# Kernel tuning notes

Measured on AMD Instinct MI355X. Metric: run time of the kernel, lower is better.

Reference implementation:

```python
import jax, jax.numpy as jnp
import numpy as np

T = 36
N_POLES = 40
LAM = 0.1
MAX_ITER = 100
TOL = 1e-4
B, P = 2, 4096


def build_dictionary(Drr, Dtheta):
    # rows i = 0..T-1; columns: [rr^i cos(i th), (-rr)^i cos(i th), rr^i sin(i th), (-rr)^i sin(i th)]
    i = jnp.arange(T, dtype=Drr.dtype)[:, None]              # [T,1]
    pr = jnp.power(Drr[None, :], i)                          # rr^i   [T,N]
    sign = jnp.power(jnp.asarray(-1.0, Drr.dtype), i)        # (-1)^i [T,1]
    c = jnp.cos(i * Dtheta[None, :])
    s = jnp.sin(i * Dtheta[None, :])
    dic = jnp.concatenate([pr * c, sign * pr * c, pr * s, sign * pr * s], axis=1)  # [T,4N]
    G = jnp.linalg.norm(dic, axis=0)                         # column norms
    G = jnp.where(G == 0, jnp.sqrt(jnp.asarray(float(T), dic.dtype)), G)
    return dic / G


def soft_shrink(v, lambd):
    return jnp.sign(v) * jnp.maximum(jnp.abs(v) - lambd, 0.0)


def fista(D, Y, lam, max_iter=MAX_ITER):
    DtD = D.T @ D                                            # [4N,4N]
    L = jnp.linalg.norm(DtD)                                 # torch.norm(DtD, 2) = Frobenius norm
    linv = 1.0 / L
    DtY = jnp.einsum('tk,btp->bkp', D, Y) * linv             # [B,4N,P]
    K = DtD.shape[0]
    A = jnp.eye(K, dtype=D.dtype) - DtD * linv               # [4N,4N]
    lambd = lam * linv
    Bb, _, Pp = DtY.shape

    # FISTA momentum coefficients are data independent -> precompute
    ts = np.ones(max_iter + 1)
    for k in range(max_iter):
        ts[k + 1] = (1 + np.sqrt(1 + 4 * ts[k] ** 2)) / 2.0
    tts = jnp.asarray((ts[:-1] - 1) / ts[1:], dtype=D.dtype)  # [max_iter]

    x0 = jnp.zeros((Bb, K, Pp), dtype=D.dtype)

    def step(carry, inputs):
        x_old, y_old, done = carry
        tt, k = inputs
        x_new = soft_shrink(jnp.einsum('kj,bjp->bkp', A, y_old) + DtY, lambd)
        y_new = x_new * (1 + tt) - x_old * tt
        # torch divides by x_old.shape[1]: P on the first check (x_old is the 2-D zeros init), 4N after
        denom = jnp.where(k == 0, float(Pp), float(K)).astype(x_new.dtype)
        conv = jnp.linalg.norm(x_old - x_new) / denom < TOL
        x_out = jnp.where(done, x_old, x_new)
        y_out = jnp.where(done, y_old, y_new)
        return (x_out, y_out, jnp.logical_or(done, conv)), None

    (x_fin, _, _), _ = jax.lax.scan(step, (x0, x0, jnp.array(False)),
                                    (tts, jnp.arange(max_iter)))
    return x_fin


def setup_inputs() -> dict:
    key = jax.random.key(0)
    k1, k2, k3 = jax.random.split(key, 3)
    Drr = jax.random.uniform(k1, (N_POLES,), dtype=jnp.float32)
    Dtheta = jax.random.uniform(k2, (N_POLES,), dtype=jnp.float32)
    x = jax.random.normal(k3, (B, T, P), dtype=jnp.float32)
    return {"Drr": Drr, "Dtheta": Dtheta, "x": x}


def reference(Drr, Dtheta, x):
    dic = build_dictionary(Drr, Dtheta)   # [T, 4N]
    sparsecode = fista(dic, x, LAM)       # [B, 4N, P]
    return sparsecode
```

## Files before the change

kernel.cpp:

```cpp
#include <hip/hip_runtime.h>
#include <hip/hip_bf16.h>
#include <hip/hip_fp16.h>

#define TT 36
#define KK 160
#define NPOLE 40
#define PP 4096
#define MAXIT 100
#define COLS 16
#define NG 2
#define NWC 4
#define NTHR 512
#define YS 168
#define GRID 256

#define WS_LINV  0
#define WS_LAMBD 1
#define WS_TTS   2
#define WS_FROB  132
#define WS_D     512
#define WS_A     6400
#define WS_AH    32000
#define WS_AL    44800

typedef float    floatx4 __attribute__((ext_vector_type(4)));
typedef short    shortx8 __attribute__((ext_vector_type(8)));
typedef _Float16 halfx8  __attribute__((ext_vector_type(8)));

__global__ void setup1(const float* __restrict__ Drr,
                       const float* __restrict__ Dth,
                       float* __restrict__ ws) {
  __shared__ float Dl[TT * KK];
  __shared__ float Gl[KK];
  const int tid = threadIdx.x;
  if (tid == 0) ws[WS_FROB] = 0.f;

  for (int idx = tid; idx < TT * KK; idx += 256) {
    int i = idx / KK, k = idx % KK;
    int g = k / NPOLE, n = k % NPOLE;
    float rr = Drr[n], th = Dth[n];
    float pr = powf(rr, (float)i);
    float ang = (float)i * th;
    float tri = (g < 2) ? cosf(ang) : sinf(ang);
    float sgn = ((g & 1) && (i & 1)) ? -1.0f : 1.0f;
    Dl[idx] = pr * tri * sgn;
  }
  __syncthreads();
  if (tid < KK) {
    float s = 0.f;
    for (int i = 0; i < TT; i++) { float v = Dl[i * KK + tid]; s += v * v; }
    float gn = sqrtf(s);
    Gl[tid] = (gn == 0.f) ? sqrtf((float)TT) : gn;
  }
  __syncthreads();
  for (int idx = tid; idx < TT * KK; idx += 256)
    ws[WS_D + idx] = Dl[idx] / Gl[idx % KK];

  if (tid == 0) {
    double ts = 1.0;
    for (int k = 0; k < MAXIT; k++) {
      double tn = (1.0 + sqrt(1.0 + 4.0 * ts * ts)) * 0.5;
      ws[WS_TTS + k] = (float)((ts - 1.0) / tn);
      ts = tn;
    }
  }
}

__global__ void setup2(float* __restrict__ ws) {
  __shared__ float red[256];
  const int a = blockIdx.x, b = threadIdx.x;
  const float* D = &ws[WS_D];
  float ss = 0.f;
  if (b < KK) {
    float s = 0.f;
    for (int t = 0; t < TT; t++) s += D[t * KK + a] * D[t * KK + b];
    ws[WS_A + a * KK + b] = s;
    ss = s * s;
  }
  red[b] = ss;
  __syncthreads();
  for (int off = 128; off > 0; off >>= 1) {
    if (b < off) red[b] += red[b + off];
    __syncthreads();
  }
  if (b == 0) atomicAdd(&ws[WS_FROB], red[0]);
}

__global__ void setup3(float* __restrict__ ws) {
  const int idx = blockIdx.x * 256 + threadIdx.x;
  const float linv = 1.0f / sqrtf(ws[WS_FROB]);
  _Float16* AHs = (_Float16*)&ws[WS_AH];
  if (idx < KK * KK) {
    int a = idx / KK, b = idx % KK;
    float av = (a == b) ? (1.0f - linv) : (0.0f - ws[WS_A + idx] * linv);
    AHs[idx] = (_Float16)av;
  }
  if (idx == 0) { ws[WS_LINV] = linv; ws[WS_LAMBD] = 0.1f * linv; }
}

__global__ __launch_bounds__(NTHR, 2)
void fista_kernel(const float* __restrict__ x, float* __restrict__ out,
                  float* __restrict__ ws) {
  __shared__ __align__(16) short ys[NG][2][COLS * YS];
  __shared__ float ttsl[MAXIT];
  __shared__ unsigned cnt[NG];

  const int tid  = threadIdx.x;
  const int w    = tid >> 6;
  const int lane = tid & 63;
  const int quad = lane >> 4;
  const int l16  = lane & 15;
  const int g    = w >> 2;
  const int v    = w & 3;
  const int bid  = blockIdx.x;
  const int bb   = (bid * 32) / PP;
  const int p0   = (bid * 32) % PP + 16 * g;
  const float linv  = ws[WS_LINV];
  const float lambd = ws[WS_LAMBD];
  const float adiag = 1.0f - linv;
  const float ahf   = (float)(_Float16)adiag;
  const float ddiag = adiag - ahf;

  int base, nrs;
  if (g == 0) { base = (v < 2) ? 48 * v : 32 * v + 32; nrs = (v < 2) ? 3 : 2; }
  else        { base = (v < 2) ? 32 * v : 48 * v - 32; nrs = (v < 2) ? 2 : 3; }

  for (int i = tid; i < MAXIT; i += NTHR) ttsl[i] = ws[WS_TTS + i];

  const _Float16* AH = (const _Float16*)&ws[WS_AH];
  halfx8 ah[3][5];
#pragma unroll
  for (int rs = 0; rs < 3; rs++) {
    if (rs < nrs) {
#pragma unroll
      for (int kc = 0; kc < 5; kc++) {
        int off = (base + 16 * rs + l16) * KK + 32 * kc + 8 * quad;
        ah[rs][kc] = *(const halfx8*)&AH[off];
      }
    }
  }

  const float* Dg = &ws[WS_D];
  float dty[3][4] = {{0.f,0.f,0.f,0.f},{0.f,0.f,0.f,0.f},{0.f,0.f,0.f,0.f}};
  {
    const float* xcol = &x[(size_t)bb * TT * PP + p0 + l16];
    for (int t = 0; t < TT; t++) {
      float xv = xcol[(size_t)t * PP];
#pragma unroll
      for (int rs = 0; rs < 3; rs++) {
        if (rs < nrs) {
          float4 d = *(const float4*)&Dg[t * KK + base + 16 * rs + 4 * quad];
          dty[rs][0] = fmaf(d.x, xv, dty[rs][0]);
          dty[rs][1] = fmaf(d.y, xv, dty[rs][1]);
          dty[rs][2] = fmaf(d.z, xv, dty[rs][2]);
          dty[rs][3] = fmaf(d.w, xv, dty[rs][3]);
        }
      }
    }
#pragma unroll
    for (int rs = 0; rs < 3; rs++)
#pragma unroll
      for (int r = 0; r < 4; r++) dty[rs][r] *= linv;
  }

  {
    int* z = (int*)&ys[0][0][0];
    for (int i = tid; i < NG * 2 * COLS * YS / 2; i += NTHR) z[i] = 0;
    if (tid < NG) cnt[tid] = 0;
  }
  float xo[3][4] = {{0.f,0.f,0.f,0.f},{0.f,0.f,0.f,0.f},{0.f,0.f,0.f,0.f}};
  float yl[3][4] = {{0.f,0.f,0.f,0.f},{0.f,0.f,0.f,0.f},{0.f,0.f,0.f,0.f}};
  float yv[3][4] = {{0.f,0.f,0.f,0.f},{0.f,0.f,0.f,0.f},{0.f,0.f,0.f,0.f}};
  __syncthreads();

  if (g == 1) __builtin_amdgcn_s_sleep(10);
  __builtin_amdgcn_s_setprio(1);

#define RD_MFMA(KC) { \
    halfx8 bh = *(const halfx8*)&yb[cb + 32 * (KC)]; \
    _Pragma("unroll") \
    for (int rs = 0; rs < 3; rs++) \
      if (rs < nrs) \
        accM[rs] = __builtin_amdgcn_mfma_f32_16x16x32_f16(ah[rs][KC], bh, accM[rs], 0, 0, 0); \
  }

#define ITER_BODY(SK, K1, K2, K3, K4) { \
    RD_MFMA(SK) \
    if (it > 0) { \
      const unsigned tgt = (unsigned)(NWC * it); \
      __builtin_amdgcn_s_setprio(0); \
      while (__atomic_load_n(&cnt[g], __ATOMIC_ACQUIRE) < tgt) \
        __builtin_amdgcn_s_sleep(1); \
      __builtin_amdgcn_s_setprio(1); \
    } \
    RD_MFMA(K1) RD_MFMA(K2) RD_MFMA(K3) RD_MFMA(K4) \
  }

  for (int it = 0; it < MAXIT; it++) {
    const short* yb = &ys[g][it & 1][0];
    const int cb = l16 * YS + 8 * quad;
    floatx4 accM[3] = {{dty[0][0], dty[0][1], dty[0][2], dty[0][3]},
                       {dty[1][0], dty[1][1], dty[1][2], dty[1][3]},
                       {dty[2][0], dty[2][1], dty[2][2], dty[2][3]}};

    if (g == 0) {
      if      (v == 0) ITER_BODY(0, 1, 2, 3, 4)
      else if (v == 1) ITER_BODY(2, 0, 1, 3, 4)
      else if (v == 2) ITER_BODY(3, 0, 1, 2, 4)
      else             ITER_BODY(4, 0, 1, 2, 3)
    } else {
      if      (v == 0) ITER_BODY(0, 1, 2, 3, 4)
      else if (v == 1) ITER_BODY(1, 0, 2, 3, 4)
      else if (v == 2) ITER_BODY(2, 0, 1, 3, 4)
      else             ITER_BODY(4, 0, 1, 2, 3)
    }

    const float tt = ttsl[it];
    short* yw = &ys[g][(it & 1) ^ 1][0];
#pragma unroll
    for (int rs = 0; rs < 3; rs++) {
      if (rs < nrs) {
        float yn[4];
#pragma unroll
        for (int r = 0; r < 4; r++) {
          float vv = fmaf(ddiag, yv[rs][r], fmaf(ahf, yl[rs][r], accM[rs][r]));
          float cl = __builtin_amdgcn_fmed3f(vv, -lambd, lambd);
          float xv = vv - cl;
          yn[r] = fmaf(tt, xv - xo[rs][r], xv);
          xo[rs][r] = xv;
        }
        _Float16 h0 = (_Float16)yn[0], h1 = (_Float16)yn[1];
        _Float16 h2 = (_Float16)yn[2], h3 = (_Float16)yn[3];
        yl[rs][0] = yn[0] - (float)h0;  yv[rs][0] = yn[0];
        yl[rs][1] = yn[1] - (float)h1;  yv[rs][1] = yn[1];
        yl[rs][2] = yn[2] - (float)h2;  yv[rs][2] = yn[2];
        yl[rs][3] = yn[3] - (float)h3;  yv[rs][3] = yn[3];
        unsigned u01 = (unsigned)__builtin_bit_cast(unsigned short, h0) |
                       ((unsigned)__builtin_bit_cast(unsigned short, h1) << 16);
        unsigned u23 = (unsigned)__builtin_bit_cast(unsigned short, h2) |
                       ((unsigned)__builtin_bit_cast(unsigned short, h3) << 16);
        const int ko = l16 * YS + base + 16 * rs + 4 * quad;
        *(uint2*)&yw[ko] = make_uint2(u01, u23);
      }
    }

    if (lane == 0) __atomic_fetch_add(&cnt[g], 1u, __ATOMIC_RELEASE);
  }

#pragma unroll
  for (int rs = 0; rs < 3; rs++) {
    if (rs < nrs) {
#pragma unroll
      for (int r = 0; r < 4; r++)
        out[((size_t)bb * KK + base + 16 * rs + 4 * quad + r) * PP + p0 + l16] = xo[rs][r];
    }
  }
}

extern "C" void kernel_launch(void* const* d_in, const int* in_sizes, int n_in,
                              void* d_out, int out_size, void* d_ws, size_t ws_size,
                              hipStream_t stream) {
  const float* Drr = (const float*)d_in[0];
  const float* Dth = (const float*)d_in[1];
  const float* x   = (const float*)d_in[2];
  float* out = (float*)d_out;
  float* ws  = (float*)d_ws;

  setup1<<<1, 256, 0, stream>>>(Drr, Dth, ws);
  setup2<<<160, 256, 0, stream>>>(ws);
  setup3<<<100, 256, 0, stream>>>(ws);
  fista_kernel<<<GRID, NTHR, 0, stream>>>(x, out, ws);
}
```

Measured before the change: 183.8 us.

## Fuse dictionary and Gram-matrix setup into the FISTA kernel, dropping setup launches

Removes the three setup kernels and has every FISTA block rebuild the normalized dictionary in shared memory. Each block computes the Frobenius norm through D·D^T tiles and its own rows of A = I - DtD/L, both using split-fp16 MFMA (hi/lo products). This removes three serialized kernel launches and the global workspace round-trips. In exchange every block repeats the setup work (transcendentals, MFMAs, extra syncs), and the split-fp16 Gram matrix may differ slightly in precision from the fp32 version.

```diff
diff --git a/kernel.cpp b/kernel.cpp
--- a/kernel.cpp
+++ b/kernel.cpp
@@ -1,5 +1,4 @@
 #include <hip/hip_runtime.h>
-#include <hip/hip_bf16.h>
 #include <hip/hip_fp16.h>
 
 #define TT 36
@@ -14,96 +13,30 @@
 #define YS 168
 #define GRID 256
 
-#define WS_LINV  0
-#define WS_LAMBD 1
-#define WS_TTS   2
-#define WS_FROB  132
-#define WS_D     512
-#define WS_A     6400
-#define WS_AH    32000
-#define WS_AL    44800
+#define SM_NT  25600
+#define SM_G   48640
+#define SM_RED 49280
+#define SM_SZ  49344
 
 typedef float    floatx4 __attribute__((ext_vector_type(4)));
-typedef short    shortx8 __attribute__((ext_vector_type(8)));
 typedef _Float16 halfx8  __attribute__((ext_vector_type(8)));
-
-__global__ void setup1(const float* __restrict__ Drr,
-                       const float* __restrict__ Dth,
-                       float* __restrict__ ws) {
-  __shared__ float Dl[TT * KK];
-  __shared__ float Gl[KK];
-  const int tid = threadIdx.x;
-  if (tid == 0) ws[WS_FROB] = 0.f;
-
-  for (int idx = tid; idx < TT * KK; idx += 256) {
-    int i = idx / KK, k = idx % KK;
-    int g = k / NPOLE, n = k % NPOLE;
-    float rr = Drr[n], th = Dth[n];
-    float pr = powf(rr, (float)i);
-    float ang = (float)i * th;
-    float tri = (g < 2) ? cosf(ang) : sinf(ang);
-    float sgn = ((g & 1) && (i & 1)) ? -1.0f : 1.0f;
-    Dl[idx] = pr * tri * sgn;
-  }
-  __syncthreads();
-  if (tid < KK) {
-    float s = 0.f;
-    for (int i = 0; i < TT; i++) { float v = Dl[i * KK + tid]; s += v * v; }
-    float gn = sqrtf(s);
-    Gl[tid] = (gn == 0.f) ? sqrtf((float)TT) : gn;
-  }
-  __syncthreads();
-  for (int idx = tid; idx < TT * KK; idx += 256)
-    ws[WS_D + idx] = Dl[idx] / Gl[idx % KK];
-
-  if (tid == 0) {
-    double ts = 1.0;
-    for (int k = 0; k < MAXIT; k++) {
-      double tn = (1.0 + sqrt(1.0 + 4.0 * ts * ts)) * 0.5;
-      ws[WS_TTS + k] = (float)((ts - 1.0) / tn);
-      ts = tn;
-    }
-  }
-}
-
-__global__ void setup2(float* __restrict__ ws) {
-  __shared__ float red[256];
-  const int a = blockIdx.x, b = threadIdx.x;
-  const float* D = &ws[WS_D];
-  float ss = 0.f;
-  if (b < KK) {
-    float s = 0.f;
-    for (int t = 0; t < TT; t++) s += D[t * KK + a] * D[t * KK + b];
-    ws[WS_A + a * KK + b] = s;
-    ss = s * s;
-  }
-  red[b] = ss;
-  __syncthreads();
-  for (int off = 128; off > 0; off >>= 1) {
-    if (b < off) red[b] += red[b + off];
-    __syncthreads();
-  }
-  if (b == 0) atomicAdd(&ws[WS_FROB], red[0]);
-}
-
-__global__ void setup3(float* __restrict__ ws) {
-  const int idx = blockIdx.x * 256 + threadIdx.x;
-  const float linv = 1.0f / sqrtf(ws[WS_FROB]);
-  _Float16* AHs = (_Float16*)&ws[WS_AH];
-  if (idx < KK * KK) {
-    int a = idx / KK, b = idx % KK;
-    float av = (a == b) ? (1.0f - linv) : (0.0f - ws[WS_A + idx] * linv);
-    AHs[idx] = (_Float16)av;
-  }
-  if (idx == 0) { ws[WS_LINV] = linv; ws[WS_LAMBD] = 0.1f * linv; }
-}
+typedef _Float16 halfx4  __attribute__((ext_vector_type(4)));
 
 __global__ __launch_bounds__(NTHR, 2)
-void fista_kernel(const float* __restrict__ x, float* __restrict__ out,
-                  float* __restrict__ ws) {
-  __shared__ __align__(16) short ys[NG][2][COLS * YS];
+void fista_kernel(const float* __restrict__ Drr, const float* __restrict__ Dth,
+                  const float* __restrict__ x, float* __restrict__ out) {
+  __shared__ __align__(16) char smem[SM_SZ];
   __shared__ float ttsl[MAXIT];
   __shared__ unsigned cnt[NG];
+
+  float*    rawD = (float*)smem;
+  _Float16* Th   = (_Float16*)smem;
+  _Float16* Tl   = Th + KK * 40;
+  _Float16* Nh   = (_Float16*)(smem + SM_NT);
+  _Float16* Nl   = Nh + TT * KK;
+  float*    Gn   = (float*)(smem + SM_G);
+  float*    red  = (float*)(smem + SM_RED);
+  short*    ysb  = (short*)smem;
 
   const int tid  = threadIdx.x;
   const int w    = tid >> 6;
@@ -115,32 +48,156 @@
   const int bid  = blockIdx.x;
   const int bb   = (bid * 32) / PP;
   const int p0   = (bid * 32) % PP + 16 * g;
-  const float linv  = ws[WS_LINV];
-  const float lambd = ws[WS_LAMBD];
+
+  int base, nrs;
+  if (g == 0) { base = (v < 2) ? 48 * v : 32 * v + 32; nrs = (v < 2) ? 3 : 2; }
+  else        { base = (v < 2) ? 32 * v : 48 * v - 32; nrs = (v < 2) ? 2 : 3; }
+
+#pragma unroll
+  for (int i = 0; i < 12; i++) {
+    int idx = tid + i * NTHR;
+    if (idx < TT * KK) {
+      int t = idx / KK, k = idx % KK;
+      int gg = k / NPOLE, n = k % NPOLE;
+      float rr = Drr[n], th = Dth[n];
+      float pr = powf(rr, (float)t);
+      float ang = (float)t * th;
+      float tri = (gg < 2) ? cosf(ang) : sinf(ang);
+      float sgn = ((gg & 1) && (t & 1)) ? -1.0f : 1.0f;
+      rawD[idx] = pr * tri * sgn;
+    }
+  }
+  if (tid == 0) {
+    double ts = 1.0;
+    for (int k = 0; k < MAXIT; k++) {
+      double tn = (1.0 + sqrt(1.0 + 4.0 * ts * ts)) * 0.5;
+      ttsl[k] = (float)((ts - 1.0) / tn);
+      ts = tn;
+    }
+  }
+  __syncthreads();
+
+  if (tid < KK) {
+    float s = 0.f;
+    for (int t = 0; t < TT; t++) { float vv = rawD[t * KK + tid]; s += vv * vv; }
+    float gn2 = sqrtf(s);
+    Gn[tid] = (gn2 == 0.f) ? sqrtf((float)TT) : gn2;
+  }
+  __syncthreads();
+
+  float dv[12];
+#pragma unroll
+  for (int i = 0; i < 12; i++) {
+    int idx = tid + i * NTHR;
+    dv[i] = (idx < TT * KK) ? rawD[idx] / Gn[idx % KK] : 0.f;
+  }
+  __syncthreads();
+
+#pragma unroll
+  for (int i = 0; i < 12; i++) {
+    int idx = tid + i * NTHR;
+    if (idx < TT * KK) {
+      int t = idx / KK, a = idx % KK;
+      float d = dv[i];
+      _Float16 h = (_Float16)d;
+      _Float16 l = (_Float16)(d - (float)h);
+      Nh[idx] = h; Nl[idx] = l;
+      Th[a * 40 + t] = h; Tl[a * 40 + t] = l;
+    }
+  }
+  if (tid < KK) {
+#pragma unroll
+    for (int e = TT; e < 40; e++) { Th[tid * 40 + e] = (_Float16)0.f; Tl[tid * 40 + e] = (_Float16)0.f; }
+  }
+  __syncthreads();
+
+#define DDT_TILE(I_, J_) { \
+    int s0 = 16 * (I_) + l16, t0 = 16 * (J_) + l16; \
+    floatx4 acc = {0.f, 0.f, 0.f, 0.f}; \
+    _Pragma("unroll") \
+    for (int ks = 0; ks < 5; ks++) { \
+      halfx8 Ahh = {}; halfx8 All = {}; halfx8 Bhh = {}; halfx8 Bll = {}; \
+      if (s0 < TT) { Ahh = *(const halfx8*)&Nh[s0 * KK + 32 * ks + 8 * quad]; \
+                     All = *(const halfx8*)&Nl[s0 * KK + 32 * ks + 8 * quad]; } \
+      if (t0 < TT) { Bhh = *(const halfx8*)&Nh[t0 * KK + 32 * ks + 8 * quad]; \
+                     Bll = *(const halfx8*)&Nl[t0 * KK + 32 * ks + 8 * quad]; } \
+      acc = __builtin_amdgcn_mfma_f32_16x16x32_f16(Ahh, Bhh, acc, 0, 0, 0); \
+      acc = __builtin_amdgcn_mfma_f32_16x16x32_f16(Ahh, Bll, acc, 0, 0, 0); \
+      acc = __builtin_amdgcn_mfma_f32_16x16x32_f16(All, Bhh, acc, 0, 0, 0); \
+    } \
+    _Pragma("unroll") \
+    for (int r2 = 0; r2 < 4; r2++) { \
+      int s2 = 16 * (I_) + 4 * quad + r2; \
+      if (s2 < TT && t0 < TT) fpart += acc[r2] * acc[r2]; \
+    } \
+  }
+
+  float fpart = 0.f;
+  DDT_TILE(w / 3, w % 3)
+  if (w == 0) DDT_TILE(2, 2)
+#pragma unroll
+  for (int off = 32; off > 0; off >>= 1) fpart += __shfl_xor(fpart, off);
+  if (lane == 0) red[w] = fpart;
+  __syncthreads();
+
+  const float frob  = ((((((red[0] + red[1]) + red[2]) + red[3]) + red[4])
+                        + red[5]) + red[6]) + red[7];
+  const float linv  = 1.0f / sqrtf(frob);
+  const float lambd = 0.1f * linv;
   const float adiag = 1.0f - linv;
   const float ahf   = (float)(_Float16)adiag;
   const float ddiag = adiag - ahf;
 
-  int base, nrs;
-  if (g == 0) { base = (v < 2) ? 48 * v : 32 * v + 32; nrs = (v < 2) ? 3 : 2; }
-  else        { base = (v < 2) ? 32 * v : 48 * v - 32; nrs = (v < 2) ? 2 : 3; }
-
-  for (int i = tid; i < MAXIT; i += NTHR) ttsl[i] = ws[WS_TTS + i];
-
-  const _Float16* AH = (const _Float16*)&ws[WS_AH];
+#define LOAD_T(HH0, LL0, HH1, LL1, ROW) \
+    halfx8 HH0 = *(const halfx8*)&Th[(ROW) * 40 + 8 * quad]; \
+    halfx8 LL0 = *(const halfx8*)&Tl[(ROW) * 40 + 8 * quad]; \
+    halfx8 HH1 = {}; halfx8 LL1 = {}; \
+    if (quad == 0) { HH1 = *(const halfx8*)&Th[(ROW) * 40 + 32]; \
+                     LL1 = *(const halfx8*)&Tl[(ROW) * 40 + 32]; }
+
   halfx8 ah[3][5];
 #pragma unroll
   for (int rs = 0; rs < 3; rs++) {
     if (rs < nrs) {
+      const int myrow = base + 16 * rs + l16;
+      LOAD_T(Bh0, Bl0, Bh1, Bl1, myrow)
 #pragma unroll
       for (int kc = 0; kc < 5; kc++) {
-        int off = (base + 16 * rs + l16) * KK + 32 * kc + 8 * quad;
-        ah[rs][kc] = *(const halfx8*)&AH[off];
+        floatx4 a0 = {0.f, 0.f, 0.f, 0.f}, a1 = {0.f, 0.f, 0.f, 0.f};
+        {
+          LOAD_T(Ah0, Al0, Ah1, Al1, 32 * kc + l16)
+          a0 = __builtin_amdgcn_mfma_f32_16x16x32_f16(Ah0, Bh0, a0, 0, 0, 0);
+          a0 = __builtin_amdgcn_mfma_f32_16x16x32_f16(Ah0, Bl0, a0, 0, 0, 0);
+          a0 = __builtin_amdgcn_mfma_f32_16x16x32_f16(Al0, Bh0, a0, 0, 0, 0);
+          a0 = __builtin_amdgcn_mfma_f32_16x16x32_f16(Ah1, Bh1, a0, 0, 0, 0);
+          a0 = __builtin_amdgcn_mfma_f32_16x16x32_f16(Ah1, Bl1, a0, 0, 0, 0);
+          a0 = __builtin_amdgcn_mfma_f32_16x16x32_f16(Al1, Bh1, a0, 0, 0, 0);
+        }
+        {
+          LOAD_T(Ch0, Cl0, Ch1, Cl1, 32 * kc + 16 + l16)
+          a1 = __builtin_amdgcn_mfma_f32_16x16x32_f16(Ch0, Bh0, a1, 0, 0, 0);
+          a1 = __builtin_amdgcn_mfma_f32_16x16x32_f16(Ch0, Bl0, a1, 0, 0, 0);
+          a1 = __builtin_amdgcn_mfma_f32_16x16x32_f16(Cl0, Bh0, a1, 0, 0, 0);
+          a1 = __builtin_amdgcn_mfma_f32_16x16x32_f16(Ch1, Bh1, a1, 0, 0, 0);
+          a1 = __builtin_amdgcn_mfma_f32_16x16x32_f16(Ch1, Bl1, a1, 0, 0, 0);
+          a1 = __builtin_amdgcn_mfma_f32_16x16x32_f16(Cl1, Bh1, a1, 0, 0, 0);
+        }
+        union { halfx8 v8; _Float16 h8[8]; } fr;
+#pragma unroll
+        for (int e = 0; e < 8; e++) {
+          int srcl = (2 * (quad & 1) + (e >> 2)) * 16 + l16;
+          float v0 = __shfl(a0[e & 3], srcl);
+          float v1 = __shfl(a1[e & 3], srcl);
+          float dd = (quad >> 1) ? v1 : v0;
+          int kpos = 32 * kc + 8 * quad + e;
+          float aval = (kpos == myrow) ? adiag : (-dd * linv);
+          fr.h8[e] = (_Float16)aval;
+        }
+        ah[rs][kc] = fr.v8;
       }
     }
   }
 
-  const float* Dg = &ws[WS_D];
   float dty[3][4] = {{0.f,0.f,0.f,0.f},{0.f,0.f,0.f,0.f},{0.f,0.f,0.f,0.f}};
   {
     const float* xcol = &x[(size_t)bb * TT * PP + p0 + l16];
@@ -149,11 +206,13 @@
 #pragma unroll
       for (int rs = 0; rs < 3; rs++) {
         if (rs < nrs) {
-          float4 d = *(const float4*)&Dg[t * KK + base + 16 * rs + 4 * quad];
-          dty[rs][0] = fmaf(d.x, xv, dty[rs][0]);
-          dty[rs][1] = fmaf(d.y, xv, dty[rs][1]);
-          dty[rs][2] = fmaf(d.z, xv, dty[rs][2]);
-          dty[rs][3] = fmaf(d.w, xv, dty[rs][3]);
+          int c0 = t * KK + base + 16 * rs + 4 * quad;
+          halfx4 dh4 = *(const halfx4*)&Nh[c0];
+          halfx4 dl4 = *(const halfx4*)&Nl[c0];
+          dty[rs][0] = fmaf((float)dh4[0] + (float)dl4[0], xv, dty[rs][0]);
+          dty[rs][1] = fmaf((float)dh4[1] + (float)dl4[1], xv, dty[rs][1]);
+          dty[rs][2] = fmaf((float)dh4[2] + (float)dl4[2], xv, dty[rs][2]);
+          dty[rs][3] = fmaf((float)dh4[3] + (float)dl4[3], xv, dty[rs][3]);
         }
       }
     }
@@ -162,9 +221,10 @@
 #pragma unroll
       for (int r = 0; r < 4; r++) dty[rs][r] *= linv;
   }
+  __syncthreads();
 
   {
-    int* z = (int*)&ys[0][0][0];
+    int* z = (int*)ysb;
     for (int i = tid; i < NG * 2 * COLS * YS / 2; i += NTHR) z[i] = 0;
     if (tid < NG) cnt[tid] = 0;
   }
@@ -197,7 +257,7 @@
   }
 
   for (int it = 0; it < MAXIT; it++) {
-    const short* yb = &ys[g][it & 1][0];
+    const short* yb = ysb + (2 * g + (it & 1)) * (COLS * YS);
     const int cb = l16 * YS + 8 * quad;
     floatx4 accM[3] = {{dty[0][0], dty[0][1], dty[0][2], dty[0][3]},
                        {dty[1][0], dty[1][1], dty[1][2], dty[1][3]},
@@ -216,7 +276,7 @@
     }
 
     const float tt = ttsl[it];
-    short* yw = &ys[g][(it & 1) ^ 1][0];
+    short* yw = ysb + (2 * g + ((it & 1) ^ 1)) * (COLS * YS);
 #pragma unroll
     for (int rs = 0; rs < 3; rs++) {
       if (rs < nrs) {
@@ -264,10 +324,7 @@
   const float* Dth = (const float*)d_in[1];
   const float* x   = (const float*)d_in[2];
   float* out = (float*)d_out;
-  float* ws  = (float*)d_ws;
-
-  setup1<<<1, 256, 0, stream>>>(Drr, Dth, ws);
-  setup2<<<160, 256, 0, stream>>>(ws);
-  setup3<<<100, 256, 0, stream>>>(ws);
-  fista_kernel<<<GRID, NTHR, 0, stream>>>(x, out, ws);
+  (void)d_ws; (void)ws_size; (void)in_sizes; (void)n_in; (void)out_size;
+
+  fista_kernel<<<GRID, NTHR, 0, stream>>>(Drr, Dth, x, out);
 }
```

Result: faster. 177.3 us (-3.5%).

## Fuse three setup kernels into one and build fp16 A inside FISTA kernel

Applied to the files above, without the earlier changes.

Merges the dictionary build, Gram matrix, and A/linv setup into a single 160-block kernel. Each block recomputes the dictionary with a sin/cos angle-addition recurrence instead of powf/cosf per element. Each block writes a per-row sum of squares, so the Frobenius atomic and the third setup kernel go away. The main kernel sums those row norms, computes linv, and converts DtD to fp16 A in registers at load time. This removes two kernel launches and their serialization, at the cost of redundant dictionary computation per block and slightly different rounding from the recurrence and __sincosf.

```diff
diff --git a/kernel.cpp b/kernel.cpp
--- a/kernel.cpp
+++ b/kernel.cpp
@@ -1,5 +1,4 @@
 #include <hip/hip_runtime.h>
-#include <hip/hip_bf16.h>
 #include <hip/hip_fp16.h>
 
 #define TT 36
@@ -14,49 +13,41 @@
 #define YS 168
 #define GRID 256
 
-#define WS_LINV  0
-#define WS_LAMBD 1
 #define WS_TTS   2
-#define WS_FROB  132
+#define WS_ROWN  160
 #define WS_D     512
 #define WS_A     6400
-#define WS_AH    32000
-#define WS_AL    44800
 
 typedef float    floatx4 __attribute__((ext_vector_type(4)));
-typedef short    shortx8 __attribute__((ext_vector_type(8)));
 typedef _Float16 halfx8  __attribute__((ext_vector_type(8)));
 
-__global__ void setup1(const float* __restrict__ Drr,
-                       const float* __restrict__ Dth,
-                       float* __restrict__ ws) {
+__global__ __launch_bounds__(256)
+void setup_kernel(const float* __restrict__ Drr, const float* __restrict__ Dth,
+                  float* __restrict__ ws) {
   __shared__ float Dl[TT * KK];
-  __shared__ float Gl[KK];
-  const int tid = threadIdx.x;
-  if (tid == 0) ws[WS_FROB] = 0.f;
-
-  for (int idx = tid; idx < TT * KK; idx += 256) {
-    int i = idx / KK, k = idx % KK;
-    int g = k / NPOLE, n = k % NPOLE;
+  __shared__ float red[256];
+  const int a = blockIdx.x, tid = threadIdx.x;
+
+  if (tid < KK) {
+    int gg = tid / NPOLE, n = tid % NPOLE;
     float rr = Drr[n], th = Dth[n];
-    float pr = powf(rr, (float)i);
-    float ang = (float)i * th;
-    float tri = (g < 2) ? cosf(ang) : sinf(ang);
-    float sgn = ((g & 1) && (i & 1)) ? -1.0f : 1.0f;
-    Dl[idx] = pr * tri * sgn;
-  }
-  __syncthreads();
-  if (tid < KK) {
-    float s = 0.f;
-    for (int i = 0; i < TT; i++) { float v = Dl[i * KK + tid]; s += v * v; }
-    float gn = sqrtf(s);
-    Gl[tid] = (gn == 0.f) ? sqrtf((float)TT) : gn;
-  }
-  __syncthreads();
-  for (int idx = tid; idx < TT * KK; idx += 256)
-    ws[WS_D + idx] = Dl[idx] / Gl[idx % KK];
-
-  if (tid == 0) {
+    float srr = (gg & 1) ? -rr : rr;
+    float sth, cth; __sincosf(th, &sth, &cth);
+    float c = 1.f, s = 0.f, pr = 1.f, ss = 0.f;
+    for (int t = 0; t < TT; t++) {
+      float val = pr * ((gg < 2) ? c : s);
+      Dl[t * KK + tid] = val;
+      ss = fmaf(val, val, ss);
+      float cn = c * cth - s * sth;
+      float sn = s * cth + c * sth;
+      c = cn; s = sn; pr *= srr;
+    }
+    float gn = sqrtf(ss);
+    gn = (gn == 0.f) ? sqrtf((float)TT) : gn;
+    float inv = 1.f / gn;
+    for (int t = 0; t < TT; t++) Dl[t * KK + tid] *= inv;
+  }
+  if (a == 0 && tid == 0) {
     double ts = 1.0;
     for (int k = 0; k < MAXIT; k++) {
       double tn = (1.0 + sqrt(1.0 + 4.0 * ts * ts)) * 0.5;
@@ -64,43 +55,30 @@
       ts = tn;
     }
   }
-}
-
-__global__ void setup2(float* __restrict__ ws) {
-  __shared__ float red[256];
-  const int a = blockIdx.x, b = threadIdx.x;
-  const float* D = &ws[WS_D];
-  float ss = 0.f;
-  if (b < KK) {
-    float s = 0.f;
-    for (int t = 0; t < TT; t++) s += D[t * KK + a] * D[t * KK + b];
-    ws[WS_A + a * KK + b] = s;
-    ss = s * s;
-  }
-  red[b] = ss;
+  __syncthreads();
+
+  if (a == 0)
+    for (int idx = tid; idx < TT * KK; idx += 256) ws[WS_D + idx] = Dl[idx];
+
+  float ss2 = 0.f;
+  if (tid < KK) {
+    float s2 = 0.f;
+    for (int t = 0; t < TT; t++) s2 = fmaf(Dl[t * KK + a], Dl[t * KK + tid], s2);
+    ws[WS_A + a * KK + tid] = s2;
+    ss2 = s2 * s2;
+  }
+  red[tid] = ss2;
   __syncthreads();
   for (int off = 128; off > 0; off >>= 1) {
-    if (b < off) red[b] += red[b + off];
+    if (tid < off) red[tid] += red[tid + off];
     __syncthreads();
   }
-  if (b == 0) atomicAdd(&ws[WS_FROB], red[0]);
-}
-
-__global__ void setup3(float* __restrict__ ws) {
-  const int idx = blockIdx.x * 256 + threadIdx.x;
-  const float linv = 1.0f / sqrtf(ws[WS_FROB]);
-  _Float16* AHs = (_Float16*)&ws[WS_AH];
-  if (idx < KK * KK) {
-    int a = idx / KK, b = idx % KK;
-    float av = (a == b) ? (1.0f - linv) : (0.0f - ws[WS_A + idx] * linv);
-    AHs[idx] = (_Float16)av;
-  }
-  if (idx == 0) { ws[WS_LINV] = linv; ws[WS_LAMBD] = 0.1f * linv; }
+  if (tid == 0) ws[WS_ROWN + a] = red[0];
 }
 
 __global__ __launch_bounds__(NTHR, 2)
 void fista_kernel(const float* __restrict__ x, float* __restrict__ out,
-                  float* __restrict__ ws) {
+                  const float* __restrict__ ws) {
   __shared__ __align__(16) short ys[NG][2][COLS * YS];
   __shared__ float ttsl[MAXIT];
   __shared__ unsigned cnt[NG];
@@ -115,8 +93,18 @@
   const int bid  = blockIdx.x;
   const int bb   = (bid * 32) / PP;
   const int p0   = (bid * 32) % PP + 16 * g;
-  const float linv  = ws[WS_LINV];
-  const float lambd = ws[WS_LAMBD];
+
+  float frob = 0.f;
+  {
+    const float* rn = &ws[WS_ROWN];
+#pragma unroll
+    for (int i = 0; i < KK; i += 4) {
+      float4 r4 = *(const float4*)&rn[i];
+      frob += ((r4.x + r4.y) + r4.z) + r4.w;
+    }
+  }
+  const float linv  = 1.0f / sqrtf(frob);
+  const float lambd = 0.1f * linv;
   const float adiag = 1.0f - linv;
   const float ahf   = (float)(_Float16)adiag;
   const float ddiag = adiag - ahf;
@@ -127,15 +115,26 @@
 
   for (int i = tid; i < MAXIT; i += NTHR) ttsl[i] = ws[WS_TTS + i];
 
-  const _Float16* AH = (const _Float16*)&ws[WS_AH];
+  const float* DtDw = &ws[WS_A];
   halfx8 ah[3][5];
 #pragma unroll
   for (int rs = 0; rs < 3; rs++) {
     if (rs < nrs) {
+      const int myrow = base + 16 * rs + l16;
+      const float* rowp = &DtDw[myrow * KK];
 #pragma unroll
       for (int kc = 0; kc < 5; kc++) {
-        int off = (base + 16 * rs + l16) * KK + 32 * kc + 8 * quad;
-        ah[rs][kc] = *(const halfx8*)&AH[off];
+        float4 d0 = *(const float4*)&rowp[32 * kc + 8 * quad];
+        float4 d1 = *(const float4*)&rowp[32 * kc + 8 * quad + 4];
+        float vals[8] = {d0.x, d0.y, d0.z, d0.w, d1.x, d1.y, d1.z, d1.w};
+        union { halfx8 v8; _Float16 h8[8]; } fr;
+#pragma unroll
+        for (int e = 0; e < 8; e++) {
+          int kpos = 32 * kc + 8 * quad + e;
+          float aval = (kpos == myrow) ? adiag : (-vals[e] * linv);
+          fr.h8[e] = (_Float16)aval;
+        }
+        ah[rs][kc] = fr.v8;
       }
     }
   }
@@ -265,9 +264,8 @@
   const float* x   = (const float*)d_in[2];
   float* out = (float*)d_out;
   float* ws  = (float*)d_ws;
-
-  setup1<<<1, 256, 0, stream>>>(Drr, Dth, ws);
-  setup2<<<160, 256, 0, stream>>>(ws);
-  setup3<<<100, 256, 0, stream>>>(ws);
+  (void)in_sizes; (void)n_in; (void)out_size; (void)ws_size;
+
+  setup_kernel<<<160, 256, 0, stream>>>(Drr, Dth, ws);
   fista_kernel<<<GRID, NTHR, 0, stream>>>(x, out, ws);
 }
```

Result: faster. 171.7 us (-6.6%).
